# Kernel tuning notes

Measured on AMD Instinct MI355X. Metric: run time of the kernel, lower is better.

Reference implementation:

```python
import jax, jax.numpy as jnp
import numpy as np

N_NODES = 100000
N_EDGES = 600000
D_IN = 128
D_HID = 128
D_OUT = 64


def setup_inputs() -> dict:
    key = jax.random.key(0)
    ks = jax.random.split(key, 6)
    x = jax.random.normal(ks[0], (N_NODES, D_IN), dtype=jnp.float32)
    edge_index = jax.random.randint(ks[1], (2, N_EDGES), 0, N_NODES, dtype=jnp.int32)
    # Glorot-ish init for GCNConv weights
    W1 = jax.random.normal(ks[2], (D_IN, D_HID), dtype=jnp.float32) * (1.0 / np.sqrt(D_IN))
    W2 = jax.random.normal(ks[3], (D_HID, D_HID), dtype=jnp.float32) * (1.0 / np.sqrt(D_HID))
    W3 = jax.random.normal(ks[4], (D_HID, D_OUT), dtype=jnp.float32) * (1.0 / np.sqrt(D_HID))
    b1 = jnp.zeros((D_HID,), dtype=jnp.float32)
    b2 = jnp.zeros((D_HID,), dtype=jnp.float32)
    b3 = jnp.zeros((D_OUT,), dtype=jnp.float32)
    return {"x": x, "edge_index": edge_index, "W1": W1, "b1": b1,
            "W2": W2, "b2": b2, "W3": W3, "b3": b3}


def reference(x, edge_index, W1, b1, W2, b2, W3, b3):
    N = x.shape[0]
    # PyG GCNConv default: add self-loops, symmetric degree normalization.
    row, col = edge_index[0], edge_index[1]
    loops = jnp.arange(N, dtype=row.dtype)
    row = jnp.concatenate([row, loops])  # source nodes
    col = jnp.concatenate([col, loops])  # destination nodes (aggregation target)
    deg = jax.ops.segment_sum(jnp.ones(row.shape, dtype=x.dtype), col, num_segments=N)
    dinv = jax.lax.rsqrt(jnp.maximum(deg, 1.0))  # deg >= 1 due to self-loops
    norm = dinv[row] * dinv[col]  # [E+N]

    def gcn_conv(h, W, b):
        hw = h @ W                                   # dense transform [N, D]
        msg = hw[row] * norm[:, None]                # gather + normalize [E+N, D]
        return jax.ops.segment_sum(msg, col, num_segments=N) + b  # scatter-add

    h = jax.nn.relu(gcn_conv(x, W1, b1))
    # dropout p=0.5 is identity in eval mode (training=False)
    h = jax.nn.relu(gcn_conv(h, W2, b2))
    h = gcn_conv(h, W3, b3)
    return jax.nn.log_softmax(h, axis=1)
```

## Files before the change

### kernel.cpp

```cpp
#include <hip/hip_runtime.h>

#define NN 100000
#define NE 600000

typedef unsigned short u16;
typedef float f32x4 __attribute__((ext_vector_type(4)));
typedef short s16x8 __attribute__((ext_vector_type(8)));
typedef u16 u16x8 __attribute__((ext_vector_type(8)));

__device__ inline u16 f2bf(float f) {
    unsigned u = __float_as_uint(f);
    return (u16)((u + 0x7FFFu + ((u >> 16) & 1u)) >> 16);
}
__device__ inline float bflo(unsigned u) { return __uint_as_float(u << 16); }
__device__ inline float bfhi(unsigned u) { return __uint_as_float(u & 0xFFFF0000u); }


__global__ void k_init_deg(int* __restrict__ deg, int n) {
    int i = blockIdx.x * 256 + threadIdx.x;
    if (i < n) deg[i] = 0;
}

__global__ void k_deg_count(const int* __restrict__ col, int* __restrict__ deg, int E) {
    int e = blockIdx.x * 256 + threadIdx.x;
    if (e < E) atomicAdd(&deg[col[e]], 1);
}

__global__ void k_dinv(const int* __restrict__ deg, float* __restrict__ dinv, int n) {
    int i = blockIdx.x * 256 + threadIdx.x;
    if (i < n) dinv[i] = rsqrtf((float)(deg[i] + 1));
}

__global__ void k_scan1(const int* __restrict__ deg, int* __restrict__ offs,
                        int* __restrict__ bsums, int n) {
    __shared__ int s[256];
    int t = threadIdx.x;
    int i = blockIdx.x * 256 + t;
    int v = (i < n) ? deg[i] : 0;
    s[t] = v;
    __syncthreads();
    for (int off = 1; off < 256; off <<= 1) {
        int x = (t >= off) ? s[t - off] : 0;
        __syncthreads();
        s[t] += x;
        __syncthreads();
    }
    if (i < n) offs[i] = s[t] - v;
    if (t == 255) bsums[blockIdx.x] = s[255];
}

__global__ void k_scan2(int* __restrict__ bsums, int nb) {
    __shared__ int s[512];
    int t = threadIdx.x;
    int v = (t < nb) ? bsums[t] : 0;
    s[t] = v;
    __syncthreads();
    for (int off = 1; off < 512; off <<= 1) {
        int x = (t >= off) ? s[t - off] : 0;
        __syncthreads();
        s[t] += x;
        __syncthreads();
    }
    if (t < nb) bsums[t] = s[t] - v;
}

__global__ void k_scan3(int* __restrict__ offs, const int* __restrict__ bsums,
                        int* __restrict__ cursor, int n) {
    int i = blockIdx.x * 256 + threadIdx.x;
    if (i < n) {
        int o = offs[i] + bsums[i >> 8];
        offs[i] = o;
        cursor[i] = o;
    }
}

__global__ void k_fill(const int* __restrict__ row, const int* __restrict__ col,
                       int* __restrict__ cursor, int* __restrict__ srcs, int E) {
    int e = blockIdx.x * 256 + threadIdx.x;
    if (e < E) {
        int p = atomicAdd(&cursor[col[e]], 1);
        srcs[p] = row[e];
    }
}


__global__ __launch_bounds__(256)
void k_cvt_bf16(const float* __restrict__ in, u16* __restrict__ out, int n8) {
    int i = blockIdx.x * 256 + threadIdx.x;
    if (i >= n8) return;
    const float4* p = (const float4*)in;
    float4 v0 = p[i * 2], v1 = p[i * 2 + 1];
    u16x8 r;
    r[0] = f2bf(v0.x); r[1] = f2bf(v0.y); r[2] = f2bf(v0.z); r[3] = f2bf(v0.w);
    r[4] = f2bf(v1.x); r[5] = f2bf(v1.y); r[6] = f2bf(v1.z); r[7] = f2bf(v1.w);
    ((u16x8*)out)[i] = r;
}


template <int DOUT>
__global__ __launch_bounds__(256)
void k_pack_w(const float* __restrict__ W, u16* __restrict__ Wp) {
    int gid = blockIdx.x * 256 + threadIdx.x;
    if (gid >= DOUT * 128) return;
    int i  = gid & 7;
    int l  = (gid >> 3) & 63;
    int kk = (gid >> 9) & 3;
    int t  = gid >> 11;
    int k = kk * 32 + ((l >> 4) << 3) + i;
    int c = t * 16 + (l & 15);
    Wp[gid] = f2bf(W[k * DOUT + c]);
}


template <int DOUT, bool OB16>
__global__ __launch_bounds__(256)
void k_gemm_mfma(const u16* __restrict__ Hb, const u16* __restrict__ Wp,
                 const float* __restrict__ dinv, void* __restrict__ Gout, int n) {
    constexpr int NT = DOUT / 16;
    int tid = threadIdx.x;
    int w = tid >> 6, l = tid & 63;
    int r0 = blockIdx.x * 64 + w * 16;
    int arow = r0 + (l & 15);
    bool avalid = arow < n;
    const s16x8* Arow = (const s16x8*)(Hb + (size_t)arow * 128);
    const s16x8* Wp8 = (const s16x8*)Wp;
    const s16x8 zero = {0, 0, 0, 0, 0, 0, 0, 0};

    f32x4 acc[NT];
#pragma unroll
    for (int t = 0; t < NT; t++) acc[t] = {0.f, 0.f, 0.f, 0.f};

#pragma unroll
    for (int kk = 0; kk < 4; kk++) {
        s16x8 a = avalid ? Arow[kk * 4 + (l >> 4)] : zero;
#pragma unroll
        for (int t = 0; t < NT; t++) {
            s16x8 b = Wp8[(t * 4 + kk) * 64 + l];
            acc[t] = __builtin_amdgcn_mfma_f32_16x16x32_bf16(a, b, acc[t], 0, 0, 0);
        }
    }

    int col = l & 15;
#pragma unroll
    for (int r = 0; r < 4; r++) {
        int gr = r0 + (l >> 4) * 4 + r;
        if (gr < n) {
            float di = dinv[gr];
#pragma unroll
            for (int t = 0; t < NT; t++) {
                float v = acc[t][r] * di;
                if (OB16)
                    ((u16*)Gout)[(size_t)gr * DOUT + t * 16 + col] = f2bf(v);
                else
                    ((float*)Gout)[(size_t)gr * DOUT + t * 16 + col] = v;
            }
        }
    }
}


__global__ __launch_bounds__(256)
void k_agg_relu(const unsigned* __restrict__ G, const int* __restrict__ offs,
                const int* __restrict__ deg, const int* __restrict__ srcs,
                const float* __restrict__ dinv, const float* __restrict__ bias,
                unsigned* __restrict__ out, int n) {
    int wid = (blockIdx.x * 256 + threadIdx.x) >> 6;
    int lane = threadIdx.x & 63;
    if (wid >= n) return;
    unsigned us = G[(size_t)wid * 64 + lane];
    float2 a0 = make_float2(bflo(us), bfhi(us));
    float2 a1 = make_float2(0.f, 0.f);
    float2 a2 = make_float2(0.f, 0.f);
    float2 a3 = make_float2(0.f, 0.f);
    int start = offs[wid];
    int cnt = deg[wid];
    int j = 0;
    for (; j + 4 <= cnt; j += 4) {
        int s0 = srcs[start + j + 0];
        int s1 = srcs[start + j + 1];
        int s2 = srcs[start + j + 2];
        int s3 = srcs[start + j + 3];
        unsigned u0 = G[(size_t)s0 * 64 + lane];
        unsigned u1 = G[(size_t)s1 * 64 + lane];
        unsigned u2 = G[(size_t)s2 * 64 + lane];
        unsigned u3 = G[(size_t)s3 * 64 + lane];
        a0.x += bflo(u0); a0.y += bfhi(u0);
        a1.x += bflo(u1); a1.y += bfhi(u1);
        a2.x += bflo(u2); a2.y += bfhi(u2);
        a3.x += bflo(u3); a3.y += bfhi(u3);
    }
    for (; j < cnt; j++) {
        int s = srcs[start + j];
        unsigned u = G[(size_t)s * 64 + lane];
        a0.x += bflo(u); a0.y += bfhi(u);
    }
    float2 acc;
    acc.x = (a0.x + a1.x) + (a2.x + a3.x);
    acc.y = (a0.y + a1.y) + (a2.y + a3.y);
    float di = dinv[wid];
    float2 bb = ((const float2*)bias)[lane];
    float rx = fmaxf(fmaf(acc.x, di, bb.x), 0.f);
    float ry = fmaxf(fmaf(acc.y, di, bb.y), 0.f);
    out[(size_t)wid * 64 + lane] = (unsigned)f2bf(rx) | ((unsigned)f2bf(ry) << 16);
}

__global__ __launch_bounds__(256)
void k_agg_softmax(const float* __restrict__ G, const int* __restrict__ offs,
                   const int* __restrict__ deg, const int* __restrict__ srcs,
                   const float* __restrict__ dinv, const float* __restrict__ bias,
                   float* __restrict__ out, int n) {
    int wid = (blockIdx.x * 256 + threadIdx.x) >> 6;
    int lane = threadIdx.x & 63;
    if (wid >= n) return;
    float a0 = G[(size_t)wid * 64 + lane];
    float a1 = 0.f, a2 = 0.f, a3 = 0.f;
    int start = offs[wid];
    int cnt = deg[wid];
    int j = 0;
    for (; j + 4 <= cnt; j += 4) {
        int s0 = srcs[start + j + 0];
        int s1 = srcs[start + j + 1];
        int s2 = srcs[start + j + 2];
        int s3 = srcs[start + j + 3];
        a0 += G[(size_t)s0 * 64 + lane];
        a1 += G[(size_t)s1 * 64 + lane];
        a2 += G[(size_t)s2 * 64 + lane];
        a3 += G[(size_t)s3 * 64 + lane];
    }
    for (; j < cnt; j++) {
        int s = srcs[start + j];
        a0 += G[(size_t)s * 64 + lane];
    }
    float acc = (a0 + a1) + (a2 + a3);
    float t = fmaf(acc, dinv[wid], bias[lane]);
    float m = t;
    for (int off = 32; off; off >>= 1) m = fmaxf(m, __shfl_xor(m, off, 64));
    float e = expf(t - m);
    float ssum = e;
    for (int off = 32; off; off >>= 1) ssum += __shfl_xor(ssum, off, 64);
    out[(size_t)wid * 64 + lane] = t - m - logf(ssum);
}


extern "C" void kernel_launch(void* const* d_in, const int* in_sizes, int n_in,
                              void* d_out, int out_size, void* d_ws, size_t ws_size,
                              hipStream_t stream) {
    const float* x  = (const float*)d_in[0];
    const int*   ei = (const int*)d_in[1];
    const int*   row = ei;
    const int*   col = ei + NE;
    const float* W1 = (const float*)d_in[2];
    const float* b1 = (const float*)d_in[3];
    const float* W2 = (const float*)d_in[4];
    const float* b2 = (const float*)d_in[5];
    const float* W3 = (const float*)d_in[6];
    const float* b3 = (const float*)d_in[7];
    float* outp = (float*)d_out;

    char* ws = (char*)d_ws;
    size_t off = 0;
    auto alloc = [&](size_t bytes) -> void* {
        void* p = (void*)(ws + off);
        off += (bytes + 255) & ~(size_t)255;
        return p;
    };
    float* dinv  = (float*)alloc((size_t)NN * 4);
    float* bufA  = (float*)alloc((size_t)NN * 128 * 4);
    u16*   bufB  = (u16*)alloc((size_t)NN * 128 * 2);
    u16*   xb    = (u16*)alloc((size_t)NN * 128 * 2);
    int*   deg   = (int*)alloc((size_t)NN * 4);
    int*   offs  = (int*)alloc((size_t)NN * 4);
    int*   cursor= (int*)alloc((size_t)NN * 4);
    int*   bsums = (int*)alloc(1024 * 4);
    int*   srcs  = (int*)alloc((size_t)NE * 4);
    u16*   wp1   = (u16*)alloc(128 * 128 * 2);
    u16*   wp2   = (u16*)alloc(128 * 128 * 2);
    u16*   wp3   = (u16*)alloc(128 * 64 * 2);

    int nbN = (NN + 255) / 256;
    int nbE = (NE + 255) / 256;

    k_init_deg <<<nbN, 256, 0, stream>>>(deg, NN);
    k_deg_count<<<nbE, 256, 0, stream>>>(col, deg, NE);
    k_dinv     <<<nbN, 256, 0, stream>>>(deg, dinv, NN);
    k_scan1    <<<nbN, 256, 0, stream>>>(deg, offs, bsums, NN);
    k_scan2    <<<1,   512, 0, stream>>>(bsums, nbN);
    k_scan3    <<<nbN, 256, 0, stream>>>(offs, bsums, cursor, NN);
    k_fill     <<<nbE, 256, 0, stream>>>(row, col, cursor, srcs, NE);

    int n8 = NN * 128 / 8;
    k_cvt_bf16 <<<(n8 + 255) / 256, 256, 0, stream>>>(x, xb, n8);
    k_pack_w<128><<<64, 256, 0, stream>>>(W1, wp1);
    k_pack_w<128><<<64, 256, 0, stream>>>(W2, wp2);
    k_pack_w<64> <<<32, 256, 0, stream>>>(W3, wp3);

    int gb = (NN + 63) / 64;
    int ab = (NN * 64 + 255) / 256;

    k_gemm_mfma<128, true><<<gb, 256, 0, stream>>>(xb, wp1, dinv, bufA, NN);
    k_agg_relu <<<ab, 256, 0, stream>>>((unsigned*)bufA, offs, deg, srcs, dinv, b1, (unsigned*)bufB, NN);
    k_gemm_mfma<128, true><<<gb, 256, 0, stream>>>(bufB, wp2, dinv, bufA, NN);
    k_agg_relu <<<ab, 256, 0, stream>>>((unsigned*)bufA, offs, deg, srcs, dinv, b2, (unsigned*)bufB, NN);
    k_gemm_mfma<64, false><<<gb, 256, 0, stream>>>(bufB, wp3, dinv, bufA, NN);
    k_agg_softmax<<<ab, 256, 0, stream>>>(bufA, offs, deg, srcs, dinv, b3, outp, NN);
}
```

Baseline: 359.2 us.

## Pack two nodes per wave in aggregation and store layer-3 GEMM output as bf16

The aggregation kernels now process two nodes per 64-lane wave, each half-wave using wider per-lane loads (uint2 for 128-wide bf16 rows, unsigned for 64-wide). The third GEMM now writes bf16 instead of fp32, which halves the gather traffic of the final softmax aggregation. The softmax reduction is restricted to 32-lane shuffles. The cost is lower precision in the last layer's gathered features and more divergence when the two nodes in a wave have different degrees.

After: 323.5 us. -9.9%, faster.

```diff
diff --git a/kernel.cpp b/kernel.cpp
--- a/kernel.cpp
+++ b/kernel.cpp
@@ -14,6 +14,9 @@
 }
 __device__ inline float bflo(unsigned u) { return __uint_as_float(u << 16); }
 __device__ inline float bfhi(unsigned u) { return __uint_as_float(u & 0xFFFF0000u); }
+__device__ inline unsigned pk(float a, float b) {
+    return (unsigned)f2bf(a) | ((unsigned)f2bf(b) << 16);
+}
 
 
 __global__ void k_init_deg(int* __restrict__ deg, int n) {
@@ -160,85 +163,109 @@
 
 
 __global__ __launch_bounds__(256)
-void k_agg_relu(const unsigned* __restrict__ G, const int* __restrict__ offs,
+void k_agg_relu(const uint2* __restrict__ G, const int* __restrict__ offs,
                 const int* __restrict__ deg, const int* __restrict__ srcs,
                 const float* __restrict__ dinv, const float* __restrict__ bias,
-                unsigned* __restrict__ out, int n) {
-    int wid = (blockIdx.x * 256 + threadIdx.x) >> 6;
-    int lane = threadIdx.x & 63;
-    if (wid >= n) return;
-    unsigned us = G[(size_t)wid * 64 + lane];
-    float2 a0 = make_float2(bflo(us), bfhi(us));
-    float2 a1 = make_float2(0.f, 0.f);
-    float2 a2 = make_float2(0.f, 0.f);
-    float2 a3 = make_float2(0.f, 0.f);
-    int start = offs[wid];
-    int cnt = deg[wid];
+                uint2* __restrict__ out, int n) {
+    int t = blockIdx.x * 256 + threadIdx.x;
+    int wv = t >> 6;
+    int lane = t & 63;
+    int hl = lane & 31;
+    int node = wv * 2 + (lane >> 5);
+    if (node >= n) return;
+
+    uint2 us = G[(size_t)node * 32 + hl];
+    float4 a0 = make_float4(bflo(us.x), bfhi(us.x), bflo(us.y), bfhi(us.y));
+    float4 a1 = make_float4(0.f, 0.f, 0.f, 0.f);
+    float4 a2 = make_float4(0.f, 0.f, 0.f, 0.f);
+    float4 a3 = make_float4(0.f, 0.f, 0.f, 0.f);
+    int start = offs[node];
+    int cnt = deg[node];
     int j = 0;
     for (; j + 4 <= cnt; j += 4) {
         int s0 = srcs[start + j + 0];
         int s1 = srcs[start + j + 1];
         int s2 = srcs[start + j + 2];
         int s3 = srcs[start + j + 3];
-        unsigned u0 = G[(size_t)s0 * 64 + lane];
-        unsigned u1 = G[(size_t)s1 * 64 + lane];
-        unsigned u2 = G[(size_t)s2 * 64 + lane];
-        unsigned u3 = G[(size_t)s3 * 64 + lane];
-        a0.x += bflo(u0); a0.y += bfhi(u0);
-        a1.x += bflo(u1); a1.y += bfhi(u1);
-        a2.x += bflo(u2); a2.y += bfhi(u2);
-        a3.x += bflo(u3); a3.y += bfhi(u3);
+        uint2 u0 = G[(size_t)s0 * 32 + hl];
+        uint2 u1 = G[(size_t)s1 * 32 + hl];
+        uint2 u2 = G[(size_t)s2 * 32 + hl];
+        uint2 u3 = G[(size_t)s3 * 32 + hl];
+        a0.x += bflo(u0.x); a0.y += bfhi(u0.x); a0.z += bflo(u0.y); a0.w += bfhi(u0.y);
+        a1.x += bflo(u1.x); a1.y += bfhi(u1.x); a1.z += bflo(u1.y); a1.w += bfhi(u1.y);
+        a2.x += bflo(u2.x); a2.y += bfhi(u2.x); a2.z += bflo(u2.y); a2.w += bfhi(u2.y);
+        a3.x += bflo(u3.x); a3.y += bfhi(u3.x); a3.z += bflo(u3.y); a3.w += bfhi(u3.y);
     }
     for (; j < cnt; j++) {
         int s = srcs[start + j];
-        unsigned u = G[(size_t)s * 64 + lane];
-        a0.x += bflo(u); a0.y += bfhi(u);
-    }
-    float2 acc;
+        uint2 u = G[(size_t)s * 32 + hl];
+        a0.x += bflo(u.x); a0.y += bfhi(u.x); a0.z += bflo(u.y); a0.w += bfhi(u.y);
+    }
+    float4 acc;
     acc.x = (a0.x + a1.x) + (a2.x + a3.x);
     acc.y = (a0.y + a1.y) + (a2.y + a3.y);
-    float di = dinv[wid];
-    float2 bb = ((const float2*)bias)[lane];
-    float rx = fmaxf(fmaf(acc.x, di, bb.x), 0.f);
-    float ry = fmaxf(fmaf(acc.y, di, bb.y), 0.f);
-    out[(size_t)wid * 64 + lane] = (unsigned)f2bf(rx) | ((unsigned)f2bf(ry) << 16);
-}
-
-__global__ __launch_bounds__(256)
-void k_agg_softmax(const float* __restrict__ G, const int* __restrict__ offs,
+    acc.z = (a0.z + a1.z) + (a2.z + a3.z);
+    acc.w = (a0.w + a1.w) + (a2.w + a3.w);
+    float di = dinv[node];
+    float4 bb = ((const float4*)bias)[hl];
+    float r0 = fmaxf(fmaf(acc.x, di, bb.x), 0.f);
+    float r1 = fmaxf(fmaf(acc.y, di, bb.y), 0.f);
+    float r2 = fmaxf(fmaf(acc.z, di, bb.z), 0.f);
+    float r3 = fmaxf(fmaf(acc.w, di, bb.w), 0.f);
+    out[(size_t)node * 32 + hl] = make_uint2(pk(r0, r1), pk(r2, r3));
+}
+
+__global__ __launch_bounds__(256)
+void k_agg_softmax(const unsigned* __restrict__ G, const int* __restrict__ offs,
                    const int* __restrict__ deg, const int* __restrict__ srcs,
                    const float* __restrict__ dinv, const float* __restrict__ bias,
-                   float* __restrict__ out, int n) {
-    int wid = (blockIdx.x * 256 + threadIdx.x) >> 6;
-    int lane = threadIdx.x & 63;
-    if (wid >= n) return;
-    float a0 = G[(size_t)wid * 64 + lane];
-    float a1 = 0.f, a2 = 0.f, a3 = 0.f;
-    int start = offs[wid];
-    int cnt = deg[wid];
+                   float2* __restrict__ out, int n) {
+    int t = blockIdx.x * 256 + threadIdx.x;
+    int wv = t >> 6;
+    int lane = t & 63;
+    int hl = lane & 31;
+    int node = wv * 2 + (lane >> 5);
+    if (node >= n) return;
+
+    unsigned us = G[(size_t)node * 32 + hl];
+    float2 a0 = make_float2(bflo(us), bfhi(us));
+    float2 a1 = make_float2(0.f, 0.f);
+    float2 a2 = make_float2(0.f, 0.f);
+    float2 a3 = make_float2(0.f, 0.f);
+    int start = offs[node];
+    int cnt = deg[node];
     int j = 0;
     for (; j + 4 <= cnt; j += 4) {
         int s0 = srcs[start + j + 0];
         int s1 = srcs[start + j + 1];
         int s2 = srcs[start + j + 2];
         int s3 = srcs[start + j + 3];
-        a0 += G[(size_t)s0 * 64 + lane];
-        a1 += G[(size_t)s1 * 64 + lane];
-        a2 += G[(size_t)s2 * 64 + lane];
-        a3 += G[(size_t)s3 * 64 + lane];
+        unsigned u0 = G[(size_t)s0 * 32 + hl];
+        unsigned u1 = G[(size_t)s1 * 32 + hl];
+        unsigned u2 = G[(size_t)s2 * 32 + hl];
+        unsigned u3 = G[(size_t)s3 * 32 + hl];
+        a0.x += bflo(u0); a0.y += bfhi(u0);
+        a1.x += bflo(u1); a1.y += bfhi(u1);
+        a2.x += bflo(u2); a2.y += bfhi(u2);
+        a3.x += bflo(u3); a3.y += bfhi(u3);
     }
     for (; j < cnt; j++) {
         int s = srcs[start + j];
-        a0 += G[(size_t)s * 64 + lane];
-    }
-    float acc = (a0 + a1) + (a2 + a3);
-    float t = fmaf(acc, dinv[wid], bias[lane]);
-    float m = t;
-    for (int off = 32; off; off >>= 1) m = fmaxf(m, __shfl_xor(m, off, 64));
-    float e = expf(t - m);
-    float ssum = e;
-    for (int off = 32; off; off >>= 1) ssum += __shfl_xor(ssum, off, 64);
-    out[(size_t)wid * 64 + lane] = t - m - logf(ssum);
+        unsigned u = G[(size_t)s * 32 + hl];
+        a0.x += bflo(u); a0.y += bfhi(u);
+    }
+    float di = dinv[node];
+    float2 bb = ((const float2*)bias)[hl];
+    float t0 = fmaf((a0.x + a1.x) + (a2.x + a3.x), di, bb.x);
+    float t1 = fmaf((a0.y + a1.y) + (a2.y + a3.y), di, bb.y);
+    float m = fmaxf(t0, t1);
+#pragma unroll
+    for (int off = 1; off < 32; off <<= 1) m = fmaxf(m, __shfl_xor(m, off, 64));
+    float e = expf(t0 - m) + expf(t1 - m);
+#pragma unroll
+    for (int off = 1; off < 32; off <<= 1) e += __shfl_xor(e, off, 64);
+    float lse = m + logf(e);
+    out[(size_t)node * 32 + hl] = make_float2(t0 - lse, t1 - lse);
 }
 
 
@@ -295,12 +322,12 @@
     k_pack_w<64> <<<32, 256, 0, stream>>>(W3, wp3);
 
     int gb = (NN + 63) / 64;
-    int ab = (NN * 64 + 255) / 256;
+    int ab2 = ((NN + 1) / 2 * 64 + 255) / 256;
 
     k_gemm_mfma<128, true><<<gb, 256, 0, stream>>>(xb, wp1, dinv, bufA, NN);
-    k_agg_relu <<<ab, 256, 0, stream>>>((unsigned*)bufA, offs, deg, srcs, dinv, b1, (unsigned*)bufB, NN);
+    k_agg_relu <<<ab2, 256, 0, stream>>>((uint2*)bufA, offs, deg, srcs, dinv, b1, (uint2*)bufB, NN);
     k_gemm_mfma<128, true><<<gb, 256, 0, stream>>>(bufB, wp2, dinv, bufA, NN);
-    k_agg_relu <<<ab, 256, 0, stream>>>((unsigned*)bufA, offs, deg, srcs, dinv, b2, (unsigned*)bufB, NN);
-    k_gemm_mfma<64, false><<<gb, 256, 0, stream>>>(bufB, wp3, dinv, bufA, NN);
-    k_agg_softmax<<<ab, 256, 0, stream>>>(bufA, offs, deg, srcs, dinv, b3, outp, NN);
-}
+    k_agg_relu <<<ab2, 256, 0, stream>>>((uint2*)bufA, offs, deg, srcs, dinv, b2, (uint2*)bufB, NN);
+    k_gemm_mfma<64, true><<<gb, 256, 0, stream>>>(bufB, wp3, dinv, bufA, NN);
+    k_agg_softmax<<<ab2, 256, 0, stream>>>((unsigned*)bufA, offs, deg, srcs, dinv, b3, (float2*)outp, NN);
+}
```
